# Optimization experiments

Hardware: AMD Instinct MI355X
Metric: run time of the kernel (lower is better)

Reference implementation:

```python
import jax, jax.numpy as jnp
import numpy as np

N_NODES = 50000
N_EDGES = 800000
IN_FEATS = 512
OUT_FEATS = 512
DROP_P = 0.1


def setup_inputs() -> dict:
    key = jax.random.key(0)
    k1, k2, k3, k4, k5 = jax.random.split(key, 5)
    x = jax.random.normal(k1, (N_NODES, IN_FEATS), dtype=jnp.float32)
    edge_w = jax.random.uniform(k2, (N_EDGES,), dtype=jnp.float32)
    W = jax.random.normal(k3, (IN_FEATS, OUT_FEATS), dtype=jnp.float32) * (1.0 / np.sqrt(IN_FEATS))
    b = jnp.zeros((OUT_FEATS,), dtype=jnp.float32)
    edge_src = jax.random.randint(k4, (N_EDGES,), 0, N_NODES, dtype=jnp.int32)
    edge_dst = jnp.sort(jax.random.randint(k5, (N_EDGES,), 0, N_NODES, dtype=jnp.int32))
    return {"x": x, "edge_w": edge_w, "W": W, "b": b,
            "edge_src": edge_src, "edge_dst": edge_dst}


def reference(x, edge_w, W, b, edge_src, edge_dst):
    # Dropout (train mode, p=0.1) with a fixed key for determinism.
    keep = jax.random.bernoulli(jax.random.key(42), 1.0 - DROP_P, x.shape)
    xd = jnp.where(keep, x / (1.0 - DROP_P), 0.0)
    # Sparse adjacency matmul: out[dst] += adj_w * x[src]  (torch.spmm(adj, x))
    msgs = xd[edge_src] * edge_w[:, None]          # [E, in_feats]
    agg = jax.ops.segment_sum(msgs, edge_dst, num_segments=N_NODES)  # [N, in_feats]
    # Linear + ReLU activation
    return jax.nn.relu(agg @ W + b)
```

## Files before the change

kernel.cpp:

```cpp
#include <hip/hip_runtime.h>
#include <hip/hip_bf16.h>
#include <stdint.h>


#define N_NODESC 50000
#define N_EDGESC 800000
#define FEATS    512
#define TOT_ELEMS (N_NODESC * FEATS)

typedef unsigned int u32;
typedef unsigned short u16;
typedef __attribute__((ext_vector_type(8))) short short8;
typedef __attribute__((ext_vector_type(4))) float floatx4;

__device__ __forceinline__ void tf_round(u32& a, u32& b, int r) {
  a += b;
  b = (b << r) | (b >> (32 - r));
  b ^= a;
}

__device__ __forceinline__ void threefry(u32& x0, u32& x1) {
  const u32 k0 = 0u, k1 = 42u, k2 = 0x1BD11BDAu ^ 0u ^ 42u;
  x0 += k0; x1 += k1;
  tf_round(x0,x1,13); tf_round(x0,x1,15); tf_round(x0,x1,26); tf_round(x0,x1,6);
  x0 += k1; x1 += k2 + 1u;
  tf_round(x0,x1,17); tf_round(x0,x1,29); tf_round(x0,x1,16); tf_round(x0,x1,24);
  x0 += k2; x1 += k0 + 2u;
  tf_round(x0,x1,13); tf_round(x0,x1,15); tf_round(x0,x1,26); tf_round(x0,x1,6);
  x0 += k0; x1 += k1 + 3u;
  tf_round(x0,x1,17); tf_round(x0,x1,29); tf_round(x0,x1,16); tf_round(x0,x1,24);
  x0 += k1; x1 += k2 + 4u;
  tf_round(x0,x1,13); tf_round(x0,x1,15); tf_round(x0,x1,26); tf_round(x0,x1,6);
  x0 += k2; x1 += k0 + 5u;
}

__device__ __forceinline__ u16 f2bf(float f) {
  u32 u = __float_as_uint(f);
  u32 r = (u + 0x7FFFu + ((u >> 16) & 1u)) >> 16;
  return (u16)r;
}

__global__ __launch_bounds__(256) void drop_kernel(const float* __restrict__ x,
                                                   u16* __restrict__ xd) {
  int t = blockIdx.x * 256 + threadIdx.x;
  int j0 = t * 4;
  float4 xv = *(const float4*)(x + j0);
  float xs[4] = {xv.x, xv.y, xv.z, xv.w};
  u16 r[4];
#pragma unroll
  for (int q = 0; q < 4; ++q) {
    u32 a = 0u, b = (u32)(j0 + q);
    threefry(a, b);
    u32 bits = a ^ b;
    float u = __uint_as_float((bits >> 9) | 0x3F800000u) - 1.0f;
    float m = (u < 0.9f) ? (1.0f / 0.9f) : 0.0f;
    r[q] = f2bf(xs[q] * m);
  }
  uint2 o;
  o.x = (u32)r[0] | ((u32)r[1] << 16);
  o.y = (u32)r[2] | ((u32)r[3] << 16);
  *(uint2*)(xd + j0) = o;
}

__global__ __launch_bounds__(256) void wconv_kernel(const float* __restrict__ W,
                                                    u16* __restrict__ WbT) {
  int t = blockIdx.x * 256 + threadIdx.x;
  int k = t >> 9, n = t & 511;
  WbT[n * 512 + k] = f2bf(W[t]);
}

__global__ __launch_bounds__(64) void agg_kernel(const u16* __restrict__ xd,
                                                 const float* __restrict__ ew,
                                                 const int* __restrict__ src,
                                                 const int* __restrict__ dst,
                                                 u16* __restrict__ agg) {
  int node = blockIdx.x;
  int lo, hi;
  { int l = 0, r = N_EDGESC;
    while (l < r) { int m = (l + r) >> 1; if (dst[m] < node) l = m + 1; else r = m; }
    lo = l; }
  { int l = lo, r = N_EDGESC;
    while (l < r) { int m = (l + r) >> 1; if (dst[m] <= node) l = m + 1; else r = m; }
    hi = l; }

  int tid = threadIdx.x;
  float acc[8] = {0.f,0.f,0.f,0.f,0.f,0.f,0.f,0.f};
  for (int e = lo; e < hi; ++e) {
    float w = ew[e];
    int s = src[e];
    uint4 v = ((const uint4*)(xd + (size_t)s * FEATS))[tid];
    u32 vv[4] = {v.x, v.y, v.z, v.w};
#pragma unroll
    for (int q = 0; q < 4; ++q) {
      acc[2*q]   += w * __uint_as_float(vv[q] << 16);
      acc[2*q+1] += w * __uint_as_float(vv[q] & 0xFFFF0000u);
    }
  }
  uint4 o;
  o.x = (u32)f2bf(acc[0]) | ((u32)f2bf(acc[1]) << 16);
  o.y = (u32)f2bf(acc[2]) | ((u32)f2bf(acc[3]) << 16);
  o.z = (u32)f2bf(acc[4]) | ((u32)f2bf(acc[5]) << 16);
  o.w = (u32)f2bf(acc[6]) | ((u32)f2bf(acc[7]) << 16);
  ((uint4*)(agg + (size_t)node * FEATS))[tid] = o;
}

#define BM 128
#define BN 128
#define BK 64

__global__ __launch_bounds__(256) void gemm_kernel(const u16* __restrict__ A,
                                                   const u16* __restrict__ BT,
                                                   const float* __restrict__ bias,
                                                   float* __restrict__ out) {
  __shared__ __align__(16) u16 Asm[BM * BK];
  __shared__ __align__(16) u16 Bsm[BN * BK];

  const int tid  = threadIdx.x;
  const int lane = tid & 63;
  const int w    = tid >> 6;
  const int m0 = blockIdx.x * BM;
  const int n0 = blockIdx.y * BN;
  const int wm = (w >> 1) * 64;
  const int wn = (w & 1) * 64;
  const int lm   = lane & 15;
  const int quad = lane >> 4;
  const int lrow = lane >> 3;
  const int lcol = (lane & 7) * 8;

  floatx4 acc[4][4];
#pragma unroll
  for (int i = 0; i < 4; ++i)
#pragma unroll
    for (int j = 0; j < 4; ++j) acc[i][j] = (floatx4)0.0f;

  for (int k0 = 0; k0 < 512; k0 += BK) {
#pragma unroll
    for (int t = 0; t < 4; ++t) {
      int chunk = w * 4 + t;
      int row = chunk * 8 + lrow;
      int gm = m0 + row;
      if (gm > N_NODESC - 1) gm = N_NODESC - 1;
      __builtin_amdgcn_global_load_lds(
          (const __attribute__((address_space(1))) void*)(A + (size_t)gm * 512 + k0 + lcol),
          (__attribute__((address_space(3))) void*)((char*)Asm + chunk * 1024),
          16, 0, 0);
      __builtin_amdgcn_global_load_lds(
          (const __attribute__((address_space(1))) void*)(BT + (size_t)(n0 + row) * 512 + k0 + lcol),
          (__attribute__((address_space(3))) void*)((char*)Bsm + chunk * 1024),
          16, 0, 0);
    }
    __syncthreads();

#pragma unroll
    for (int kk = 0; kk < BK; kk += 32) {
      short8 af[4], bfr[4];
#pragma unroll
      for (int i = 0; i < 4; ++i)
        af[i] = *(const short8*)(Asm + (wm + i * 16 + lm) * BK + kk + quad * 8);
#pragma unroll
      for (int j = 0; j < 4; ++j)
        bfr[j] = *(const short8*)(Bsm + (wn + j * 16 + lm) * BK + kk + quad * 8);
#pragma unroll
      for (int i = 0; i < 4; ++i)
#pragma unroll
        for (int j = 0; j < 4; ++j)
          acc[i][j] = __builtin_amdgcn_mfma_f32_16x16x32_bf16(af[i], bfr[j], acc[i][j], 0, 0, 0);
    }
    __syncthreads();
  }

#pragma unroll
  for (int j = 0; j < 4; ++j) {
    int col = n0 + wn + j * 16 + lm;
    float bv = bias[col];
#pragma unroll
    for (int i = 0; i < 4; ++i) {
      int row0 = m0 + wm + i * 16 + quad * 4;
#pragma unroll
      for (int r = 0; r < 4; ++r) {
        int row = row0 + r;
        if (row < N_NODESC) {
          float v = acc[i][j][r] + bv;
          out[(size_t)row * 512 + col] = v > 0.0f ? v : 0.0f;
        }
      }
    }
  }
}

extern "C" void kernel_launch(void* const* d_in, const int* in_sizes, int n_in,
                              void* d_out, int out_size, void* d_ws, size_t ws_size,
                              hipStream_t stream) {
  const float* x  = (const float*)d_in[0];
  const float* ew = (const float*)d_in[1];
  const float* W  = (const float*)d_in[2];
  const float* b  = (const float*)d_in[3];
  const int* esrc = (const int*)d_in[4];
  const int* edst = (const int*)d_in[5];
  float* out = (float*)d_out;

  char* ws = (char*)d_ws;
  u16* xd  = (u16*)ws;
  u16* agg = (u16*)(ws + (size_t)TOT_ELEMS * 2);
  u16* WbT = (u16*)(ws + (size_t)TOT_ELEMS * 4);
  (void)ew; (void)ws_size; (void)n_in; (void)in_sizes; (void)out_size;

  hipLaunchKernelGGL(drop_kernel,  dim3(TOT_ELEMS / (256 * 4)), dim3(256), 0, stream, x, xd);
  hipLaunchKernelGGL(wconv_kernel, dim3((512 * 512) / 256),     dim3(256), 0, stream, W, WbT);
  hipLaunchKernelGGL(agg_kernel,   dim3(N_NODESC),              dim3(64),  0, stream,
                     xd, ew, esrc, edst, agg);
  hipLaunchKernelGGL(gemm_kernel,  dim3((N_NODESC + BM - 1) / BM, 512 / BN), dim3(256), 0, stream,
                     agg, WbT, b, out);
}
```

Measured before the change: 411.8 us.

## Build CSR row pointers once and unroll edge gather loop by four

A new kernel builds a CSR row-pointer array from the sorted destination indices. Each aggregation block now reads its edge range with two loads instead of running two binary searches over the full edge array. The gather loop is also unrolled four edges at a time so several row loads are in flight at once. The cost is one extra small kernel launch, more workspace, and higher register use in the aggregation kernel.

```diff
diff --git a/kernel.cpp b/kernel.cpp
--- a/kernel.cpp
+++ b/kernel.cpp
@@ -69,33 +69,57 @@
   WbT[n * 512 + k] = f2bf(W[t]);
 }
 
+__global__ __launch_bounds__(256) void rowptr_kernel(const int* __restrict__ dst,
+                                                     int* __restrict__ rowptr) {
+  int e = blockIdx.x * 256 + threadIdx.x;
+  if (e > N_EDGESC) return;
+  int d  = (e < N_EDGESC) ? dst[e] : N_NODESC;
+  int pd = (e > 0) ? dst[e - 1] : -1;
+  for (int n = pd + 1; n <= d; ++n) rowptr[n] = e;
+}
+
 __global__ __launch_bounds__(64) void agg_kernel(const u16* __restrict__ xd,
                                                  const float* __restrict__ ew,
                                                  const int* __restrict__ src,
-                                                 const int* __restrict__ dst,
+                                                 const int* __restrict__ rowptr,
                                                  u16* __restrict__ agg) {
   int node = blockIdx.x;
-  int lo, hi;
-  { int l = 0, r = N_EDGESC;
-    while (l < r) { int m = (l + r) >> 1; if (dst[m] < node) l = m + 1; else r = m; }
-    lo = l; }
-  { int l = lo, r = N_EDGESC;
-    while (l < r) { int m = (l + r) >> 1; if (dst[m] <= node) l = m + 1; else r = m; }
-    hi = l; }
-
+  int lo = rowptr[node];
+  int hi = rowptr[node + 1];
   int tid = threadIdx.x;
   float acc[8] = {0.f,0.f,0.f,0.f,0.f,0.f,0.f,0.f};
-  for (int e = lo; e < hi; ++e) {
+
+  int e = lo;
+  for (; e + 4 <= hi; e += 4) {
+    uint4 v[4]; float w[4];
+#pragma unroll
+    for (int q = 0; q < 4; ++q) {
+      int s = src[e + q];
+      w[q] = ew[e + q];
+      v[q] = ((const uint4*)(xd + (size_t)s * FEATS))[tid];
+    }
+#pragma unroll
+    for (int q = 0; q < 4; ++q) {
+      u32 a[4] = {v[q].x, v[q].y, v[q].z, v[q].w};
+#pragma unroll
+      for (int p = 0; p < 4; ++p) {
+        acc[2*p]   += w[q] * __uint_as_float(a[p] << 16);
+        acc[2*p+1] += w[q] * __uint_as_float(a[p] & 0xFFFF0000u);
+      }
+    }
+  }
+  for (; e < hi; ++e) {
     float w = ew[e];
     int s = src[e];
     uint4 v = ((const uint4*)(xd + (size_t)s * FEATS))[tid];
-    u32 vv[4] = {v.x, v.y, v.z, v.w};
-#pragma unroll
-    for (int q = 0; q < 4; ++q) {
-      acc[2*q]   += w * __uint_as_float(vv[q] << 16);
-      acc[2*q+1] += w * __uint_as_float(vv[q] & 0xFFFF0000u);
-    }
-  }
+    u32 a[4] = {v.x, v.y, v.z, v.w};
+#pragma unroll
+    for (int p = 0; p < 4; ++p) {
+      acc[2*p]   += w * __uint_as_float(a[p] << 16);
+      acc[2*p+1] += w * __uint_as_float(a[p] & 0xFFFF0000u);
+    }
+  }
+
   uint4 o;
   o.x = (u32)f2bf(acc[0]) | ((u32)f2bf(acc[1]) << 16);
   o.y = (u32)f2bf(acc[2]) | ((u32)f2bf(acc[3]) << 16);
@@ -200,15 +224,18 @@
   float* out = (float*)d_out;
 
   char* ws = (char*)d_ws;
-  u16* xd  = (u16*)ws;
-  u16* agg = (u16*)(ws + (size_t)TOT_ELEMS * 2);
-  u16* WbT = (u16*)(ws + (size_t)TOT_ELEMS * 4);
-  (void)ew; (void)ws_size; (void)n_in; (void)in_sizes; (void)out_size;
-
-  hipLaunchKernelGGL(drop_kernel,  dim3(TOT_ELEMS / (256 * 4)), dim3(256), 0, stream, x, xd);
-  hipLaunchKernelGGL(wconv_kernel, dim3((512 * 512) / 256),     dim3(256), 0, stream, W, WbT);
-  hipLaunchKernelGGL(agg_kernel,   dim3(N_NODESC),              dim3(64),  0, stream,
-                     xd, ew, esrc, edst, agg);
-  hipLaunchKernelGGL(gemm_kernel,  dim3((N_NODESC + BM - 1) / BM, 512 / BN), dim3(256), 0, stream,
+  u16* xd    = (u16*)ws;
+  u16* agg   = (u16*)(ws + (size_t)TOT_ELEMS * 2);
+  u16* WbT   = (u16*)(ws + (size_t)TOT_ELEMS * 4);
+  int* rowp  = (int*)(ws + (size_t)TOT_ELEMS * 4 + 512 * 512 * 2);
+  (void)ws_size; (void)n_in; (void)in_sizes; (void)out_size;
+
+  hipLaunchKernelGGL(drop_kernel,   dim3(TOT_ELEMS / (256 * 4)), dim3(256), 0, stream, x, xd);
+  hipLaunchKernelGGL(wconv_kernel,  dim3((512 * 512) / 256),     dim3(256), 0, stream, W, WbT);
+  hipLaunchKernelGGL(rowptr_kernel, dim3((N_EDGESC + 1 + 255) / 256), dim3(256), 0, stream,
+                     edst, rowp);
+  hipLaunchKernelGGL(agg_kernel,    dim3(N_NODESC),              dim3(64),  0, stream,
+                     xd, ew, esrc, rowp, agg);
+  hipLaunchKernelGGL(gemm_kernel,   dim3((N_NODESC + BM - 1) / BM, 512 / BN), dim3(256), 0, stream,
                      agg, WbT, b, out);
 }
```

Result: faster. 395.5 us (-4.0%).
